# Performance work log

Measured on AMD Instinct MI355X. Metric: run time of the kernel, lower is better.

## Reference

```python
import jax, jax.numpy as jnp
import numpy as np
from jax import lax

PRE_NMS_TOPK = 6000
POST_NMS_TOPK = 1000
NMS_THRESH = 0.7
MIN_SIZE = 16.0


def setup_inputs() -> dict:
    key = jax.random.key(0)
    k1, k2, k3, k4 = jax.random.split(key, 4)
    N = 2_000_000
    H, W = 800, 1216
    images = jnp.zeros((1, H, W, 3), jnp.float32)  # only shape is used
    origin_sizes = jnp.ones((1, 2), jnp.float32)   # unused by forward math
    # synthesize valid anchor boxes (x1,y1,x2,y2) inside the image
    cxy = jax.random.uniform(k1, (N, 2), jnp.float32) * jnp.array([W, H], jnp.float32)
    wh = MIN_SIZE + jax.random.uniform(k2, (N, 2), jnp.float32) * 256.0
    anchors = jnp.concatenate([cxy - 0.5 * wh, cxy + 0.5 * wh], axis=1)
    bbox_deltas = 0.1 * jax.random.normal(k3, (N, 4), jnp.float32)
    logits = jax.random.normal(k4, (N, 1), jnp.float32)
    return {"images": images, "origin_sizes": origin_sizes, "anchors": anchors,
            "bbox_deltas": bbox_deltas, "logits": logits}


def _greedy_nms(boxes, valid_init):
    # boxes: [K,4] sorted by descending score; valid_init: [K] bool
    x1, y1, x2, y2 = boxes[:, 0], boxes[:, 1], boxes[:, 2], boxes[:, 3]
    areas = (x2 - x1) * (y2 - y1)

    def body(i, state):
        valid, keep = state
        idx = jnp.argmax(valid)          # first unsuppressed (boxes are score-sorted)
        ok = valid[idx]
        b = boxes[idx]
        xx1 = jnp.maximum(b[0], x1)
        yy1 = jnp.maximum(b[1], y1)
        xx2 = jnp.minimum(b[2], x2)
        yy2 = jnp.minimum(b[3], y2)
        inter = jnp.maximum(xx2 - xx1, 0.0) * jnp.maximum(yy2 - yy1, 0.0)
        iou = inter / (areas[idx] + areas - inter)
        valid = jnp.where(ok, valid & (iou <= NMS_THRESH), valid)  # self iou==1 suppresses idx
        keep = keep.at[i].set(jnp.where(ok, idx.astype(jnp.int32), -1))
        return valid, keep

    keep0 = jnp.full((POST_NMS_TOPK,), -1, jnp.int32)
    _, keep = lax.fori_loop(0, POST_NMS_TOPK, body, (valid_init, keep0))
    return keep


def reference(images, origin_sizes, anchors, bbox_deltas, logits):
    # ---- bbox delta decode ----
    wa = anchors[:, 2] - anchors[:, 0]
    ha = anchors[:, 3] - anchors[:, 1]
    xa = anchors[:, 0] + 0.5 * wa
    ya = anchors[:, 1] + 0.5 * ha
    x = bbox_deltas[:, 0] * wa + xa
    y = bbox_deltas[:, 1] * ha + ya
    w = jnp.exp(bbox_deltas[:, 2]) * wa
    h = jnp.exp(bbox_deltas[:, 3]) * ha
    # ---- clip to image ----
    height = jnp.float32(images.shape[1])
    width = jnp.float32(images.shape[2])
    x1 = jnp.clip(x - 0.5 * w, 0.0, width - 1.0)
    y1 = jnp.clip(y - 0.5 * h, 0.0, height - 1.0)
    x2 = jnp.clip(x + 0.5 * w, 0.0, width - 1.0)
    y2 = jnp.clip(y + 0.5 * h, 0.0, height - 1.0)
    proposals = jnp.stack([x1, y1, x2, y2], axis=1)  # [N,4]
    # ---- min-size filter (as score masking to stay static-shape) ----
    ok = ((x2 - x1) >= MIN_SIZE) & ((y2 - y1) >= MIN_SIZE)
    scores = jnp.where(ok, jax.nn.sigmoid(logits[:, 0]), -1.0)
    # ---- pre-NMS top-k ----
    top_scores, top_idx = lax.top_k(scores, PRE_NMS_TOPK)
    top_props = proposals[top_idx]           # [K,4]
    valid = top_scores >= 0.0
    # ---- greedy NMS (indices only; not differentiable) ----
    keep = _greedy_nms(lax.stop_gradient(top_props), valid)  # [post_nms_topk]
    kept_mask = keep >= 0
    out = jnp.where(kept_mask[:, None], top_props[jnp.maximum(keep, 0)], 0.0)
    return out  # [POST_NMS_TOPK, 4], zero rows where fewer than topk survive
```

## Files before the change

### kernel.cpp

```cpp
#include <hip/hip_runtime.h>
#include <hip/hip_bf16.h>
#include <stdint.h>

typedef unsigned int uint;
typedef unsigned long long ull;

#define NPRE   6000
#define NPOST  1000
#define NW     94
#define MCAP   16384
#define IMG_W  1216.0f
#define IMG_H  800.0f

#define WS_KEYS    0
#define WS_HIST    8000000
#define WS_STATE   8001024
#define WS_K64     8001088
#define WS_IDX     8132160
#define WS_RANK    8197696
#define WS_SORTED  8263232
#define WS_MASK    8359488

__device__ __forceinline__ float exp_ref(float x) { return (float)exp((double)x); }

__device__ __forceinline__ float sigmoid_ref(float x) {
#pragma clang fp contract(off)
    float e = exp_ref(-x);
    float d = 1.0f + e;
    return 1.0f / d;
}

__device__ __forceinline__ bool decode_box(float4 a, float4 d,
                                           float& x1, float& y1, float& x2, float& y2) {
#pragma clang fp contract(off)
    float wa = a.z - a.x;
    float ha = a.w - a.y;
    float xa = a.x + 0.5f * wa;
    float ya = a.y + 0.5f * ha;
    float x  = d.x * wa + xa;
    float y  = d.y * ha + ya;
    float w  = exp_ref(d.z) * wa;
    float h  = exp_ref(d.w) * ha;
    x1 = fminf(fmaxf(x - 0.5f * w, 0.0f), IMG_W - 1.0f);
    y1 = fminf(fmaxf(y - 0.5f * h, 0.0f), IMG_H - 1.0f);
    x2 = fminf(fmaxf(x + 0.5f * w, 0.0f), IMG_W - 1.0f);
    y2 = fminf(fmaxf(y + 0.5f * h, 0.0f), IMG_H - 1.0f);
    return (x2 - x1 >= 16.0f) && (y2 - y1 >= 16.0f);
}

__device__ __forceinline__ bool sup_check(float ax1, float ay1, float ax2, float ay2, float aar,
                                          float bx1, float by1, float bx2, float by2, float bar) {
#pragma clang fp contract(off)
    float xx1 = fmaxf(ax1, bx1);
    float yy1 = fmaxf(ay1, by1);
    float xx2 = fminf(ax2, bx2);
    float yy2 = fminf(ay2, by2);
    float inter = fmaxf(xx2 - xx1, 0.0f) * fmaxf(yy2 - yy1, 0.0f);
    float uni = (aar + bar) - inter;
    return !(inter / uni <= 0.7f);
}

__global__ void k_init(uint* hist, uint* state, uint* rank, float4* sorted) {
    int t = blockIdx.x * blockDim.x + threadIdx.x;
    for (int i = t; i < MCAP; i += gridDim.x * blockDim.x) rank[i] = 0;
    if (t < 256) hist[t] = 0;
    if (t < 16)  state[t] = 0;
    if (t < 16)  sorted[NPRE + t] = make_float4(0.f, 0.f, 0.f, 0.f);
}

__global__ void k_decode_hist(const float4* __restrict__ A, const float4* __restrict__ D,
                              const float* __restrict__ L, uint* __restrict__ keys,
                              uint* __restrict__ hist, int N) {
    __shared__ uint h[256];
    int t = threadIdx.x;
    h[t] = 0;
    __syncthreads();
    for (int i = blockIdx.x * blockDim.x + t; i < N; i += gridDim.x * blockDim.x) {
        float x1, y1, x2, y2;
        bool ok = decode_box(A[i], D[i], x1, y1, x2, y2);
        uint key = 0u;
        if (ok) {
            float s = sigmoid_ref(L[i]);
            key = __float_as_uint(s) | 0x80000000u;
        }
        keys[i] = key;
        if ((key >> 24) == 0xBFu) atomicAdd(&h[(key >> 16) & 0xFFu], 1u);
    }
    __syncthreads();
    uint v = h[t];
    if (v) atomicAdd(&hist[t], v);
}

__global__ __launch_bounds__(256) void k_compact16(const uint* __restrict__ keys, int N,
                                                   const uint* __restrict__ hist, uint* state,
                                                   ull* __restrict__ K64, int* __restrict__ idxArr) {
    __shared__ uint S[256];
    __shared__ uint t8s;
    int t = threadIdx.x;
    if (t == 0) t8s = 0;
    S[t] = hist[t];
    __syncthreads();
    for (int off = 1; off < 256; off <<= 1) {
        uint v = S[t] + ((t + off < 256) ? S[t + off] : 0u);
        __syncthreads();
        S[t] = v;
        __syncthreads();
    }
    uint Sincl = S[t];
    uint Sexcl = (t < 255) ? S[t + 1] : 0u;
    if (Sincl >= NPRE && Sexcl < NPRE) t8s = (uint)t;
    __syncthreads();
    uint T16 = 0xBF00u | t8s;

    int i = blockIdx.x * blockDim.x + t;
    int lane = t & 63;
    uint key = (i < N) ? keys[i] : 0u;
    bool push = (i < N) && ((key >> 16) >= T16);
    ull b = __ballot(push);
    if (!b) return;
    int ldr = __builtin_ctzll(b);
    uint base = 0;
    if (lane == ldr) base = atomicAdd(&state[1], (uint)__builtin_popcountll(b));
    base = (uint)__shfl((int)base, ldr, 64);
    if (push) {
        uint p = base + (uint)__builtin_popcountll(b & ((1ull << lane) - 1ull));
        if (p < MCAP) {
            K64[p] = ((ull)key << 32) | (uint)(~(uint)i);
            idxArr[p] = i;
        }
    }
}

__global__ __launch_bounds__(256) void k_rank(const ull* __restrict__ K64,
                                              const uint* __restrict__ state,
                                              uint* __restrict__ rank) {
    __shared__ ull tile[256];
    int M = (int)min(state[1], (uint)MCAP);
    if ((int)blockIdx.x * 256 >= M) return;
    int i = blockIdx.x * 256 + threadIdx.x;
    int W = (M + 7) / 8;
    int c0 = blockIdx.y * W;
    int c1 = min(c0 + W, M);
    ull mine = (i < M) ? K64[i] : 0ull;
    uint cnt = 0;
    for (int base = c0; base < c1; base += 256) {
        int j = base + threadIdx.x;
        tile[threadIdx.x] = (j < c1) ? K64[j] : 0ull;
        __syncthreads();
        int lim = min(256, c1 - base);
        for (int t = 0; t < lim; ++t) cnt += (tile[t] > mine);
        __syncthreads();
    }
    if (i < M && cnt) atomicAdd(&rank[i], cnt);
}

__global__ void k_scatter(const float4* __restrict__ A, const float4* __restrict__ D,
                          const uint* __restrict__ state, const uint* __restrict__ rank,
                          const int* __restrict__ idxArr, float4* __restrict__ sorted) {
    int i = blockIdx.x * blockDim.x + threadIdx.x;
    int M = (int)min(state[1], (uint)MCAP);
    if (i >= M) return;
    uint r = rank[i];
    if (r >= NPRE) return;
    int idx = idxArr[i];
    float x1, y1, x2, y2;
    decode_box(A[idx], D[idx], x1, y1, x2, y2);
    sorted[r] = make_float4(x1, y1, x2, y2);
}

__global__ __launch_bounds__(64) void k_mask(const float4* __restrict__ sorted,
                                             ull* __restrict__ mask) {
#pragma clang fp contract(off)
    if (blockIdx.x <= blockIdx.y) return;
    __shared__ float4 cb[64];
    __shared__ float  ca[64];
    int cw = blockIdx.x, rc = blockIdx.y, t = threadIdx.x;
    float4 b = sorted[cw * 64 + t];
    cb[t] = b;
    ca[t] = (b.z - b.x) * (b.w - b.y);
    __syncthreads();
    int row = rc * 64 + t;
    float4 rb = sorted[row];
    float  ra = (rb.z - rb.x) * (rb.w - rb.y);
    ull bits = 0;
    for (int j = 0; j < 64; ++j)
        if (sup_check(rb.x, rb.y, rb.z, rb.w, ra,
                      cb[j].x, cb[j].y, cb[j].z, cb[j].w, ca[j]))
            bits |= 1ull << j;
    mask[(size_t)row * NW + cw] = bits;
}

__global__ __launch_bounds__(1024) void k_nms(const float4* __restrict__ sorted,
                                              const ull* __restrict__ mask,
                                              float* __restrict__ out) {
    int tid = threadIdx.x, lane = tid & 63, w = tid >> 6;
    __shared__ float kx1[NPOST], ky1[NPOST], kx2[NPOST], ky2[NPOST];
    __shared__ int   fIdx[64];
    __shared__ float cbx1[2][64], cby1[2][64], cbx2[2][64], cby2[2][64], cbar[2][64];
    __shared__ ull   intra[64];
    __shared__ uint  remLo[NW], remHi[NW];
    __shared__ int   kcS, nfS;

    for (int i = tid; i < NW; i += 1024) { remLo[i] = 0; remHi[i] = 0; }
    if (tid < 64) {
#pragma clang fp contract(off)
        float4 b = sorted[tid];
        cbx1[0][tid] = b.x; cby1[0][tid] = b.y; cbx2[0][tid] = b.z; cby2[0][tid] = b.w;
        cbar[0][tid] = (b.z - b.x) * (b.w - b.y);
    }
    if (tid == 0) { kcS = 0; nfS = 0; }
    __syncthreads();

    int kc = 0, nf = 0;
    for (int c = 0; c < NW; ++c) {
        int cur = c & 1;
        int nw2 = NW - c;
        int pairs = nf * nw2;
        for (int p = tid; p < pairs; p += 1024) {
            int k  = p / nw2;
            int ww = c + (p - k * nw2);
            ull m = mask[(size_t)fIdx[k] * NW + ww];
            uint lo = (uint)m, hi = (uint)(m >> 32);
            if (lo) atomicOr(&remLo[ww], lo);
            if (hi) atomicOr(&remHi[ww], hi);
        }
        bool pf = (w == 15) && (c + 1 < NW);
        float4 nb;
        if (pf) nb = sorted[(c + 1) * 64 + lane];
        float cx1 = cbx1[cur][lane], cy1 = cby1[cur][lane];
        float cx2 = cbx2[cur][lane], cy2 = cby2[cur][lane], car = cbar[cur][lane];
        for (int i2 = 0; i2 < 4; ++i2) {
            int r = w * 4 + i2;
            bool sup = sup_check(cbx1[cur][r], cby1[cur][r], cbx2[cur][r], cby2[cur][r],
                                 cbar[cur][r], cx1, cy1, cx2, cy2, car);
            ull bal = __ballot(sup);
            if (lane == 0) intra[r] = bal;
        }
        if (pf) {
#pragma clang fp contract(off)
            int nxt = cur ^ 1;
            cbx1[nxt][lane] = nb.x; cby1[nxt][lane] = nb.y;
            cbx2[nxt][lane] = nb.z; cby2[nxt][lane] = nb.w;
            cbar[nxt][lane] = (nb.z - nb.x) * (nb.w - nb.y);
        }
        __syncthreads();
        if (w == 0) {
            ull myrow = intra[lane];
            ull rm = ((ull)remHi[c] << 32) | (ull)remLo[c];
            if (c == NW - 1) rm |= 0xFFFF000000000000ull;
            ull alive = ~rm;
            uint rlo = (uint)myrow, rhi = (uint)(myrow >> 32);
            ull keptbits = 0;
            int kcl = kc;
            while (alive && kcl < NPOST) {
                int j = __builtin_ctzll(alive);
                int js = __builtin_amdgcn_readfirstlane(j);
                keptbits |= 1ull << js;
                kcl++;
                uint mlo = __builtin_amdgcn_readlane(rlo, js);
                uint mhi = __builtin_amdgcn_readlane(rhi, js);
                alive &= ~(((ull)mhi << 32) | (ull)mlo);
                alive &= ~(1ull << js);
            }
            if ((keptbits >> lane) & 1ull) {
                int r = kc + __builtin_popcountll(keptbits & ((1ull << lane) - 1ull));
                kx1[r] = cx1; ky1[r] = cy1; kx2[r] = cx2; ky2[r] = cy2;
                fIdx[r - kc] = c * 64 + lane;
            }
            if (lane == 0) { kcS = kcl; nfS = kcl - kc; }
        }
        __syncthreads();
        kc = kcS; nf = nfS;
        if (kc >= NPOST) break;
    }
    float4* o4 = (float4*)out;
    for (int r = tid; r < NPOST; r += 1024) {
        float4 b = make_float4(0.f, 0.f, 0.f, 0.f);
        if (r < kc) b = make_float4(kx1[r], ky1[r], kx2[r], ky2[r]);
        o4[r] = b;
    }
}

extern "C" void kernel_launch(void* const* d_in, const int* in_sizes, int n_in,
                              void* d_out, int out_size, void* d_ws, size_t ws_size,
                              hipStream_t stream) {
    const float4* A = (const float4*)d_in[2];
    const float4* D = (const float4*)d_in[3];
    const float*  L = (const float*)d_in[4];
    int N = in_sizes[4];

    char* ws = (char*)d_ws;
    uint*   keys   = (uint*)(ws + WS_KEYS);
    uint*   hist   = (uint*)(ws + WS_HIST);
    uint*   state  = (uint*)(ws + WS_STATE);
    ull*    K64    = (ull*)(ws + WS_K64);
    int*    idxArr = (int*)(ws + WS_IDX);
    uint*   rank   = (uint*)(ws + WS_RANK);
    float4* sorted = (float4*)(ws + WS_SORTED);
    ull*    mask   = (ull*)(ws + WS_MASK);
    float*  out    = (float*)d_out;

    int nblk = (N + 255) / 256;

    k_init<<<16, 1024, 0, stream>>>(hist, state, rank, sorted);
    k_decode_hist<<<2048, 256, 0, stream>>>(A, D, L, keys, hist, N);
    k_compact16<<<nblk, 256, 0, stream>>>(keys, N, hist, state, K64, idxArr);
    k_rank<<<dim3(64, 8), 256, 0, stream>>>(K64, state, rank);
    k_scatter<<<64, 256, 0, stream>>>(A, D, state, rank, idxArr, sorted);
    k_mask<<<dim3(NW, NW), 64, 0, stream>>>(sorted, mask);
    k_nms<<<1, 1024, 0, stream>>>(sorted, mask, out);
}
```

Baseline: 272.9 us.

## Fuse rank and scatter kernels, dropping the split-column rank atomics

```diff
diff --git a/kernel.cpp b/kernel.cpp
--- a/kernel.cpp
+++ b/kernel.cpp
@@ -17,7 +17,6 @@
 #define WS_STATE   8001024
 #define WS_K64     8001088
 #define WS_IDX     8132160
-#define WS_RANK    8197696
 #define WS_SORTED  8263232
 #define WS_MASK    8359488
 
@@ -60,12 +59,11 @@
     return !(inter / uni <= 0.7f);
 }
 
-__global__ void k_init(uint* hist, uint* state, uint* rank, float4* sorted) {
+__global__ void k_init(uint* hist, uint* state, float4* sorted) {
     int t = blockIdx.x * blockDim.x + threadIdx.x;
-    for (int i = t; i < MCAP; i += gridDim.x * blockDim.x) rank[i] = 0;
     if (t < 256) hist[t] = 0;
-    if (t < 16)  state[t] = 0;
-    if (t < 16)  sorted[NPRE + t] = make_float4(0.f, 0.f, 0.f, 0.f);
+    if (t >= 256 && t < 272) state[t - 256] = 0;
+    if (t >= 272 && t < 288) sorted[NPRE + (t - 272)] = make_float4(0.f, 0.f, 0.f, 0.f);
 }
 
 __global__ void k_decode_hist(const float4* __restrict__ A, const float4* __restrict__ D,
@@ -131,41 +129,32 @@
     }
 }
 
-__global__ __launch_bounds__(256) void k_rank(const ull* __restrict__ K64,
-                                              const uint* __restrict__ state,
-                                              uint* __restrict__ rank) {
+__global__ __launch_bounds__(256) void k_rankscatter(const ull* __restrict__ K64,
+                                                     const uint* __restrict__ state,
+                                                     const int* __restrict__ idxArr,
+                                                     const float4* __restrict__ A,
+                                                     const float4* __restrict__ D,
+                                                     float4* __restrict__ sorted) {
     __shared__ ull tile[256];
     int M = (int)min(state[1], (uint)MCAP);
     if ((int)blockIdx.x * 256 >= M) return;
     int i = blockIdx.x * 256 + threadIdx.x;
-    int W = (M + 7) / 8;
-    int c0 = blockIdx.y * W;
-    int c1 = min(c0 + W, M);
     ull mine = (i < M) ? K64[i] : 0ull;
     uint cnt = 0;
-    for (int base = c0; base < c1; base += 256) {
+    for (int base = 0; base < M; base += 256) {
         int j = base + threadIdx.x;
-        tile[threadIdx.x] = (j < c1) ? K64[j] : 0ull;
-        __syncthreads();
-        int lim = min(256, c1 - base);
+        tile[threadIdx.x] = (j < M) ? K64[j] : 0ull;
+        __syncthreads();
+        int lim = min(256, M - base);
         for (int t = 0; t < lim; ++t) cnt += (tile[t] > mine);
         __syncthreads();
     }
-    if (i < M && cnt) atomicAdd(&rank[i], cnt);
-}
-
-__global__ void k_scatter(const float4* __restrict__ A, const float4* __restrict__ D,
-                          const uint* __restrict__ state, const uint* __restrict__ rank,
-                          const int* __restrict__ idxArr, float4* __restrict__ sorted) {
-    int i = blockIdx.x * blockDim.x + threadIdx.x;
-    int M = (int)min(state[1], (uint)MCAP);
-    if (i >= M) return;
-    uint r = rank[i];
-    if (r >= NPRE) return;
-    int idx = idxArr[i];
-    float x1, y1, x2, y2;
-    decode_box(A[idx], D[idx], x1, y1, x2, y2);
-    sorted[r] = make_float4(x1, y1, x2, y2);
+    if (i < M && cnt < NPRE) {
+        int idx = idxArr[i];
+        float x1, y1, x2, y2;
+        decode_box(A[idx], D[idx], x1, y1, x2, y2);
+        sorted[cnt] = make_float4(x1, y1, x2, y2);
+    }
 }
 
 __global__ __launch_bounds__(64) void k_mask(const float4* __restrict__ sorted,
@@ -295,18 +284,16 @@
     uint*   state  = (uint*)(ws + WS_STATE);
     ull*    K64    = (ull*)(ws + WS_K64);
     int*    idxArr = (int*)(ws + WS_IDX);
-    uint*   rank   = (uint*)(ws + WS_RANK);
     float4* sorted = (float4*)(ws + WS_SORTED);
     ull*    mask   = (ull*)(ws + WS_MASK);
     float*  out    = (float*)d_out;
 
     int nblk = (N + 255) / 256;
 
-    k_init<<<16, 1024, 0, stream>>>(hist, state, rank, sorted);
+    k_init<<<1, 512, 0, stream>>>(hist, state, sorted);
     k_decode_hist<<<2048, 256, 0, stream>>>(A, D, L, keys, hist, N);
     k_compact16<<<nblk, 256, 0, stream>>>(keys, N, hist, state, K64, idxArr);
-    k_rank<<<dim3(64, 8), 256, 0, stream>>>(K64, state, rank);
-    k_scatter<<<64, 256, 0, stream>>>(A, D, state, rank, idxArr, sorted);
+    k_rankscatter<<<64, 256, 0, stream>>>(K64, state, idxArr, A, D, sorted);
     k_mask<<<dim3(NW, NW), 64, 0, stream>>>(sorted, mask);
     k_nms<<<1, 1024, 0, stream>>>(sorted, mask, out);
 }
```

After: 355.9 us. 30.4% more time.
